# Kernel optimization log

Hardware: AMD Instinct MI355X
Metric: run time of the kernel (lower is better)

Reference implementation:

```python
import jax, jax.numpy as jnp
import numpy as np

N = 20000      # nodes
E = 320000     # edges (before self loops)
C = 128        # hidesize (in = out channels)
H = 5          # attention heads
NEG_SLOPE = 0.2
EPS = 1e-16


def setup_inputs() -> dict:
    key = jax.random.key(0)
    k1, k2, k3, k4, k5, k6 = jax.random.split(key, 6)
    features = jax.random.normal(k1, (N, C), dtype=jnp.float32)
    edge_index = jax.random.randint(k2, (2, E), 0, N, dtype=jnp.int64)
    # GATConv parameters: shared linear for src/dst, per-head attention vectors, bias
    W = jax.random.normal(k3, (C, H * C), dtype=jnp.float32) * (1.0 / np.sqrt(C))
    att_src = jax.random.normal(k4, (H, C), dtype=jnp.float32) * 0.1
    att_dst = jax.random.normal(k5, (H, C), dtype=jnp.float32) * 0.1
    bias = jax.random.normal(k6, (C,), dtype=jnp.float32) * 0.1
    return {"features": features, "W": W, "att_src": att_src,
            "att_dst": att_dst, "bias": bias, "edge_index": edge_index}


def _gat_forward(features, W, att_src, att_dst, bias, edge_index):
    n = features.shape[0]
    # add_self_loops=True: append (i -> i) for every node
    loop = jnp.arange(n, dtype=edge_index.dtype)
    src = jnp.concatenate([edge_index[0], loop])  # message source j
    dst = jnp.concatenate([edge_index[1], loop])  # aggregation target i

    h = (features @ W).reshape(n, H, C)           # [N,H,C] projected per head
    alpha_src = jnp.sum(h * att_src, axis=-1)     # [N,H]
    alpha_dst = jnp.sum(h * att_dst, axis=-1)     # [N,H]

    e = alpha_src[src] + alpha_dst[dst]           # [E',H]
    e = jax.nn.leaky_relu(e, negative_slope=NEG_SLOPE)

    # segment softmax over edges grouped by destination node
    e_max = jax.ops.segment_max(e, dst, num_segments=n)   # [N,H]
    e = jnp.exp(e - e_max[dst])
    denom = jax.ops.segment_sum(e, dst, num_segments=n)   # [N,H]
    alpha = e / (denom[dst] + EPS)                         # [E',H]

    msg = h[src] * alpha[:, :, None]                       # [E',H,C]
    out = jax.ops.segment_sum(msg, dst, num_segments=n)    # [N,H,C]
    out = out.mean(axis=1) + bias                          # concat=False -> head mean
    return features + out                                  # use_residual=True


def reference(features, W, att_src, att_dst, bias, edge_index):
    return _gat_forward(features, W, att_src, att_dst, bias, edge_index)
```

## Files before the change

### kernel.cpp

```cpp
#include <hip/hip_runtime.h>
#include <hip/hip_bf16.h>
#include <stdint.h>

#define C_DIM 128
#define H_DIM 5
#define PAD_DEG 64

typedef __bf16 bf16x8 __attribute__((ext_vector_type(8)));
typedef float f32x4 __attribute__((ext_vector_type(4)));
typedef float f32x2 __attribute__((ext_vector_type(2)));

static __device__ __forceinline__ ushort f2bf(float x) {
    __hip_bfloat16 b = __float2bfloat16(x);
    return *reinterpret_cast<ushort*>(&b);
}

__global__ __launch_bounds__(256) void zero_kernel(int* __restrict__ cnt, int N4) {
    int idx = blockIdx.x * 256 + threadIdx.x;
    if (idx < N4) *reinterpret_cast<int4*>(cnt + idx * 4) = make_int4(0, 0, 0, 0);
}

__global__ __launch_bounds__(256) void prep0_kernel(
    const float* __restrict__ F, const float* __restrict__ W,
    const float* __restrict__ att_src, const float* __restrict__ att_dst,
    ushort* __restrict__ Abf, ushort* __restrict__ Bt, float* __restrict__ Wa,
    const int* __restrict__ srcArr, const int* __restrict__ dstArr,
    int* __restrict__ cnt, int* __restrict__ colp,
    int Bw, int Bb, int Bc, int N, int E) {
    int b = blockIdx.x;
    int tid = threadIdx.x;
    if (b < Bw) {
        int t = b * 256 + tid;
        if (t < C_DIM * 10) {
            int k = t / 10, j = t % 10;
            int h = j % 5;
            const float* att = ((j < 5) ? att_src : att_dst) + h * C_DIM;
            const float* w = W + (size_t)k * (H_DIM * C_DIM) + h * C_DIM;
            float sum = 0.f;
#pragma unroll 8
            for (int c = 0; c < C_DIM; ++c) sum = fmaf(w[c], att[c], sum);
            Wa[k * 10 + j] = sum;
        }
    } else if (b < Bw + Bb) {
        int t = (b - Bw) * 256 + tid;
        if (t < 640 * 128) {
            int c = t >> 7, k = t & 127;
            Bt[t] = f2bf(W[(size_t)k * 640 + c]);
        }
    } else if (b < Bw + Bb + Bc) {
        int t = (b - Bw - Bb) * 256 + tid;
        if (t < N * 16) {
            const float4* f4 = reinterpret_cast<const float4*>(F) + (size_t)t * 2;
            float4 v0 = f4[0], v1 = f4[1];
            float vv[8] = {v0.x, v0.y, v0.z, v0.w, v1.x, v1.y, v1.z, v1.w};
            ushort u[8];
#pragma unroll
            for (int i = 0; i < 8; ++i) u[i] = f2bf(vv[i]);
            *reinterpret_cast<uint4*>(Abf + (size_t)t * 8) = *reinterpret_cast<uint4*>(u);
        }
    } else {
        int e = (b - Bw - Bb - Bc) * 256 + tid;
        if (e < E + N) {
            int s, i;
            if (e < E) { s = srcArr[e]; i = dstArr[e]; }
            else       { s = e - E;    i = s; }
            int pos = atomicAdd(&cnt[i], 1);
            if (pos < PAD_DEG) colp[(size_t)i * PAD_DEG + pos] = s;
        }
    }
}

__global__ __launch_bounds__(256) void gemm_alpha_kernel(
    const ushort* __restrict__ Abf, const ushort* __restrict__ Bt,
    unsigned char* __restrict__ Hout,
    const float* __restrict__ F, const float* __restrict__ Wa,
    float* __restrict__ asrc, float* __restrict__ adst,
    int NBG, int NRB, int N) {
    __shared__ char smem[52224];
    int tid = threadIdx.x;
    if ((int)blockIdx.x < NBG) {
        ushort (*As)[136] = reinterpret_cast<ushort(*)[136]>(smem);
        ushort (*Bs)[136] = reinterpret_cast<ushort(*)[136]>(smem + 128 * 136 * 2);
        int by = blockIdx.x % NRB;
        int bx = blockIdx.x / NRB;
        int row0 = by * 128, col0 = bx * 64;
        int seg = tid & 15, rb = tid >> 4;
#pragma unroll
        for (int p = 0; p < 8; ++p) {
            int r = rb + p * 16;
            int gr = row0 + r;
            uint4 v = make_uint4(0u, 0u, 0u, 0u);
            if (gr < N) v = *reinterpret_cast<const uint4*>(Abf + (size_t)gr * 128 + seg * 8);
            *reinterpret_cast<uint4*>(&As[r][seg * 8]) = v;
        }
#pragma unroll
        for (int p = 0; p < 4; ++p) {
            int r = rb + p * 16;
            uint4 v = *reinterpret_cast<const uint4*>(Bt + (size_t)(col0 + r) * 128 + seg * 8);
            *reinterpret_cast<uint4*>(&Bs[r][seg * 8]) = v;
        }
        __syncthreads();
        int wave = tid >> 6, lane = tid & 63;
        int wr = (wave & 1) * 64;
        int wc = (wave >> 1) * 32;
        int lm = lane & 15, lk = (lane >> 4) * 8;
        f32x4 acc[4][2] = {};
#pragma unroll
        for (int kk = 0; kk < 4; ++kk) {
            int k = kk * 32 + lk;
            bf16x8 a[4], bvec[2];
#pragma unroll
            for (int m = 0; m < 4; ++m)
                a[m] = *reinterpret_cast<const bf16x8*>(&As[wr + m * 16 + lm][k]);
#pragma unroll
            for (int n = 0; n < 2; ++n)
                bvec[n] = *reinterpret_cast<const bf16x8*>(&Bs[wc + n * 16 + lm][k]);
#pragma unroll
            for (int m = 0; m < 4; ++m)
#pragma unroll
                for (int n = 0; n < 2; ++n)
                    acc[m][n] = __builtin_amdgcn_mfma_f32_16x16x32_bf16(a[m], bvec[n], acc[m][n], 0, 0, 0);
        }
        int r4 = (lane >> 4) * 4;
#pragma unroll
        for (int m = 0; m < 4; ++m) {
#pragma unroll
            for (int r = 0; r < 4; ++r) {
                int grow = row0 + wr + m * 16 + r4 + r;
                if (grow < N) {
                    int pk = __builtin_amdgcn_cvt_pk_fp8_f32(acc[m][0][r], acc[m][1][r], 0, false);
                    unsigned char* rowp = Hout + (size_t)grow * 640 + col0 + wc;
                    rowp[lm]      = (unsigned char)(pk & 0xff);
                    rowp[16 + lm] = (unsigned char)((pk >> 8) & 0xff);
                }
            }
        }
    } else {
        float (*f_lds)[132] = reinterpret_cast<float(*)[132]>(smem);
        float* wa_lds = reinterpret_cast<float*>(smem + 16 * 132 * 4);
        int node0 = ((int)blockIdx.x - NBG) * 16;
#pragma unroll
        for (int t = 0; t < 2; ++t) {
            int idx = tid + t * 256;
            int n = idx >> 5, c4 = idx & 31;
            int node = node0 + n;
            float4 v = make_float4(0.f, 0.f, 0.f, 0.f);
            if (node < N) v = *(reinterpret_cast<const float4*>(F) + (size_t)node * 32 + c4);
            f_lds[n][c4 * 4 + 0] = v.x;
            f_lds[n][c4 * 4 + 1] = v.y;
            f_lds[n][c4 * 4 + 2] = v.z;
            f_lds[n][c4 * 4 + 3] = v.w;
        }
#pragma unroll
        for (int t = 0; t < 5; ++t) {
            int idx = tid + t * 256;
            if (idx < 1280) wa_lds[idx] = Wa[idx];
        }
        __syncthreads();
        if (tid < 160) {
            int n = tid / 10, j = tid % 10;
            int node = node0 + n;
            if (node < N) {
                float sum = 0.f;
#pragma unroll 8
                for (int k = 0; k < C_DIM; ++k) sum = fmaf(f_lds[n][k], wa_lds[k * 10 + j], sum);
                if (j < 5) asrc[node * 5 + j] = sum;
                else       adst[node * 5 + (j - 5)] = sum;
            }
        }
    }
}

__global__ __launch_bounds__(256) void gat_aggregate(
    const int* __restrict__ cnt, const int* __restrict__ colp,
    const float* __restrict__ asrc, const float* __restrict__ adst,
    const unsigned char* __restrict__ h8,
    const float* __restrict__ features, const float* __restrict__ bias,
    float* __restrict__ out, int N) {
    int node = blockIdx.x * 4 + (threadIdx.x >> 6);
    if (node >= N) return;
    int lane = threadIdx.x & 63;
    int g = lane >> 4, m = lane & 15;
    float adg = adst[node * 5 + g];
    float ad4 = adst[node * 5 + 4];
    const int offA = g * 128 + m * 8;
    const int offB = 512 + lane * 2;
    int deg = cnt[node];
    if (deg > PAD_DEG) deg = PAD_DEG;
    const int* cp = colp + (size_t)node * PAD_DEG;
    float accG[8] = {};
    float acc4a = 0.f, acc4b = 0.f;
    float sg = 0.f, s4 = 0.f;
    int p = 0;
    for (; p + 4 <= deg; p += 4) {
        int jj[4];
#pragma unroll
        for (int b = 0; b < 4; ++b) jj[b] = cp[p + b];
        uint2 q[4]; ushort q4[4];
#pragma unroll
        for (int b = 0; b < 4; ++b) {
            const unsigned char* hp = h8 + (size_t)jj[b] * 640;
            q[b]  = *reinterpret_cast<const uint2*>(hp + offA);
            q4[b] = *reinterpret_cast<const ushort*>(hp + offB);
        }
#pragma unroll
        for (int b = 0; b < 4; ++b) {
            float eg = asrc[jj[b] * 5 + g] + adg;
            float e4 = asrc[jj[b] * 5 + 4] + ad4;
            eg = (eg > 0.f) ? eg : 0.2f * eg;
            e4 = (e4 > 0.f) ? e4 : 0.2f * e4;
            float wg = __expf(eg), w4 = __expf(e4);
            sg += wg; s4 += w4;
            f32x2 x01 = __builtin_amdgcn_cvt_pk_f32_fp8((int)q[b].x, false);
            f32x2 x23 = __builtin_amdgcn_cvt_pk_f32_fp8((int)q[b].x, true);
            f32x2 x45 = __builtin_amdgcn_cvt_pk_f32_fp8((int)q[b].y, false);
            f32x2 x67 = __builtin_amdgcn_cvt_pk_f32_fp8((int)q[b].y, true);
            accG[0] = fmaf(wg, x01[0], accG[0]);
            accG[1] = fmaf(wg, x01[1], accG[1]);
            accG[2] = fmaf(wg, x23[0], accG[2]);
            accG[3] = fmaf(wg, x23[1], accG[3]);
            accG[4] = fmaf(wg, x45[0], accG[4]);
            accG[5] = fmaf(wg, x45[1], accG[5]);
            accG[6] = fmaf(wg, x67[0], accG[6]);
            accG[7] = fmaf(wg, x67[1], accG[7]);
            f32x2 y = __builtin_amdgcn_cvt_pk_f32_fp8((int)q4[b], false);
            acc4a = fmaf(w4, y[0], acc4a);
            acc4b = fmaf(w4, y[1], acc4b);
        }
    }
    for (; p < deg; ++p) {
        int j = cp[p];
        float eg = asrc[j * 5 + g] + adg;
        float e4 = asrc[j * 5 + 4] + ad4;
        eg = (eg > 0.f) ? eg : 0.2f * eg;
        e4 = (e4 > 0.f) ? e4 : 0.2f * e4;
        float wg = __expf(eg), w4 = __expf(e4);
        sg += wg; s4 += w4;
        const unsigned char* hp = h8 + (size_t)j * 640;
        uint2 q = *reinterpret_cast<const uint2*>(hp + offA);
        ushort q4 = *reinterpret_cast<const ushort*>(hp + offB);
        f32x2 x01 = __builtin_amdgcn_cvt_pk_f32_fp8((int)q.x, false);
        f32x2 x23 = __builtin_amdgcn_cvt_pk_f32_fp8((int)q.x, true);
        f32x2 x45 = __builtin_amdgcn_cvt_pk_f32_fp8((int)q.y, false);
        f32x2 x67 = __builtin_amdgcn_cvt_pk_f32_fp8((int)q.y, true);
        accG[0] = fmaf(wg, x01[0], accG[0]);
        accG[1] = fmaf(wg, x01[1], accG[1]);
        accG[2] = fmaf(wg, x23[0], accG[2]);
        accG[3] = fmaf(wg, x23[1], accG[3]);
        accG[4] = fmaf(wg, x45[0], accG[4]);
        accG[5] = fmaf(wg, x45[1], accG[5]);
        accG[6] = fmaf(wg, x67[0], accG[6]);
        accG[7] = fmaf(wg, x67[1], accG[7]);
        f32x2 y = __builtin_amdgcn_cvt_pk_f32_fp8((int)q4, false);
        acc4a = fmaf(w4, y[0], acc4a);
        acc4b = fmaf(w4, y[1], acc4b);
    }
    float invg = 1.f / (sg + 1e-16f);
    float r[8];
#pragma unroll
    for (int e = 0; e < 8; ++e) r[e] = accG[e] * invg;
#pragma unroll
    for (int e = 0; e < 8; ++e) r[e] += __shfl_xor(r[e], 16, 64);
#pragma unroll
    for (int e = 0; e < 8; ++e) r[e] += __shfl_xor(r[e], 32, 64);
    float inv4 = 1.f / (s4 + 1e-16f);
#pragma unroll
    for (int i = 0; i < 8; ++i) {
        int srcl = 4 * m + (i >> 1);
        float h4 = __shfl((i & 1) ? acc4b : acc4a, srcl, 64);
        r[i] = fmaf(h4, inv4, r[i]);
    }
    if (g == 0) {
        int c0 = m * 8;
        size_t base = (size_t)node * 128 + c0;
        float4 f0 = *reinterpret_cast<const float4*>(features + base);
        float4 f1 = *reinterpret_cast<const float4*>(features + base + 4);
        float4 b0 = *reinterpret_cast<const float4*>(bias + c0);
        float4 b1 = *reinterpret_cast<const float4*>(bias + c0 + 4);
        float4 o0, o1;
        o0.x = f0.x + b0.x + 0.2f * r[0];
        o0.y = f0.y + b0.y + 0.2f * r[1];
        o0.z = f0.z + b0.z + 0.2f * r[2];
        o0.w = f0.w + b0.w + 0.2f * r[3];
        o1.x = f1.x + b1.x + 0.2f * r[4];
        o1.y = f1.y + b1.y + 0.2f * r[5];
        o1.z = f1.z + b1.z + 0.2f * r[6];
        o1.w = f1.w + b1.w + 0.2f * r[7];
        *reinterpret_cast<float4*>(out + base) = o0;
        *reinterpret_cast<float4*>(out + base + 4) = o1;
    }
}

static inline char* bump(char*& p, size_t bytes) {
    char* r = p;
    p += (bytes + 255) & ~(size_t)255;
    return r;
}

extern "C" void kernel_launch(void* const* d_in, const int* in_sizes, int n_in,
                              void* d_out, int out_size, void* d_ws, size_t ws_size,
                              hipStream_t stream) {
    const float* features = (const float*)d_in[0];
    const float* W        = (const float*)d_in[1];
    const float* att_src  = (const float*)d_in[2];
    const float* att_dst  = (const float*)d_in[3];
    const float* bias     = (const float*)d_in[4];
    const int*   edges    = (const int*)d_in[5];

    const int N = in_sizes[0] / C_DIM;
    const int E = in_sizes[5] / 2;
    const int EN = E + N;
    const int* srcArr = edges;
    const int* dstArr = edges + E;

    char* p = (char*)d_ws;
    float* Wa     = (float*)bump(p, C_DIM * 10 * sizeof(float));
    float* asrc   = (float*)bump(p, (size_t)N * 5 * sizeof(float));
    float* adst   = (float*)bump(p, (size_t)N * 5 * sizeof(float));
    unsigned char* h8 = (unsigned char*)bump(p, (size_t)N * 640);
    ushort* Abf   = (ushort*)bump(p, (size_t)N * C_DIM * sizeof(ushort));
    ushort* Bt    = (ushort*)bump(p, 640 * 128 * sizeof(ushort));
    int* cnt      = (int*)bump(p, (size_t)N * sizeof(int));
    int* colp     = (int*)bump(p, (size_t)N * PAD_DEG * sizeof(int));

    float* out = (float*)d_out;

    const int N4 = (N + 3) / 4;
    zero_kernel<<<(N4 + 255) / 256, 256, 0, stream>>>(cnt, N4);
    const int Bw = (C_DIM * 10 + 255) / 256;
    const int Bb = (640 * 128 + 255) / 256;
    const int Bc = (N * 16 + 255) / 256;
    const int G0 = Bw + Bb + Bc + (EN + 255) / 256;
    prep0_kernel<<<G0, 256, 0, stream>>>(features, W, att_src, att_dst, Abf, Bt, Wa,
                                         srcArr, dstArr, cnt, colp, Bw, Bb, Bc, N, E);
    const int NRB = (N + 127) / 128;
    const int NBG = NRB * 10;
    const int G1 = NBG + (N + 15) / 16;
    gemm_alpha_kernel<<<G1, 256, 0, stream>>>(Abf, Bt, h8, features, Wa, asrc, adst,
                                              NBG, NRB, N);
    gat_aggregate<<<(N + 3) / 4, 256, 0, stream>>>(cnt, colp, asrc, adst, h8, features,
                                                   bias, out, N);
}
```

Baseline: 90.00 us.

## Split each node's edge list across two wavefronts and combine via LDS

The aggregation kernel now gives each destination node two wavefronts instead of one. Each wave processes about half of the neighbor list, and the second wave writes its partial accumulators and softmax sums to shared memory for the first wave to merge before normalization. This doubles the parallelism and memory-level parallelism available to the latency-bound gather over neighbors, at the cost of a block-wide barrier, LDS traffic, and twice as many blocks.

Result: no change. 89.96 us (-0.1%).

```diff
diff --git a/kernel.cpp b/kernel.cpp
--- a/kernel.cpp
+++ b/kernel.cpp
@@ -177,22 +177,33 @@
     const unsigned char* __restrict__ h8,
     const float* __restrict__ features, const float* __restrict__ bias,
     float* __restrict__ out, int N) {
-    int node = blockIdx.x * 4 + (threadIdx.x >> 6);
-    if (node >= N) return;
+    __shared__ float comb[2][64][13];
+    int wave = threadIdx.x >> 6;
+    int nodeLocal = wave >> 1;
+    int sub = wave & 1;
+    int node = blockIdx.x * 2 + nodeLocal;
     int lane = threadIdx.x & 63;
     int g = lane >> 4, m = lane & 15;
-    float adg = adst[node * 5 + g];
-    float ad4 = adst[node * 5 + 4];
+    bool valid = node < N;
+    float adg = 0.f, ad4 = 0.f;
+    int deg = 0;
+    if (valid) {
+        adg = adst[node * 5 + g];
+        ad4 = adst[node * 5 + 4];
+        deg = cnt[node];
+        if (deg > PAD_DEG) deg = PAD_DEG;
+    }
     const int offA = g * 128 + m * 8;
     const int offB = 512 + lane * 2;
-    int deg = cnt[node];
-    if (deg > PAD_DEG) deg = PAD_DEG;
     const int* cp = colp + (size_t)node * PAD_DEG;
+    int h0 = ((deg + 7) >> 3) << 2;
+    if (h0 > deg) h0 = deg;
+    int p = sub ? h0 : 0;
+    int pend = sub ? deg : h0;
     float accG[8] = {};
     float acc4a = 0.f, acc4b = 0.f;
     float sg = 0.f, s4 = 0.f;
-    int p = 0;
-    for (; p + 4 <= deg; p += 4) {
+    for (; p + 4 <= pend; p += 4) {
         int jj[4];
 #pragma unroll
         for (int b = 0; b < 4; ++b) jj[b] = cp[p + b];
@@ -228,7 +239,7 @@
             acc4b = fmaf(w4, y[1], acc4b);
         }
     }
-    for (; p < deg; ++p) {
+    for (; p < pend; ++p) {
         int j = cp[p];
         float eg = asrc[j * 5 + g] + adg;
         float e4 = asrc[j * 5 + 4] + ad4;
@@ -255,6 +266,20 @@
         acc4a = fmaf(w4, y[0], acc4a);
         acc4b = fmaf(w4, y[1], acc4b);
     }
+    if (sub == 1) {
+        float* cb = comb[nodeLocal][lane];
+#pragma unroll
+        for (int e = 0; e < 8; ++e) cb[e] = accG[e];
+        cb[8] = acc4a; cb[9] = acc4b; cb[10] = sg; cb[11] = s4;
+    }
+    __syncthreads();
+    if (sub == 1 || !valid) return;
+    {
+        const float* cb = comb[nodeLocal][lane];
+#pragma unroll
+        for (int e = 0; e < 8; ++e) accG[e] += cb[e];
+        acc4a += cb[8]; acc4b += cb[9]; sg += cb[10]; s4 += cb[11];
+    }
     float invg = 1.f / (sg + 1e-16f);
     float r[8];
 #pragma unroll
@@ -338,6 +363,6 @@
     const int G1 = NBG + (N + 15) / 16;
     gemm_alpha_kernel<<<G1, 256, 0, stream>>>(Abf, Bt, h8, features, Wa, asrc, adst,
                                               NBG, NRB, N);
-    gat_aggregate<<<(N + 3) / 4, 256, 0, stream>>>(cnt, colp, asrc, adst, h8, features,
+    gat_aggregate<<<(N + 1) / 2, 256, 0, stream>>>(cnt, colp, asrc, adst, h8, features,
                                                    bias, out, N);
 }
```
